# Kernel tuning notes

Hardware: AMD Instinct MI355X
Metric: run time of the kernel (lower is better)

The kernel has to match this reference:

```python
import jax, jax.numpy as jnp
import numpy as np

# RPE constants from the source: pix_per_patch=200//16, alpha=12, beta=24, gamma=96, num_buckets=49
ALPHA, BETA, GAMMA, PPP = 12.0, 24.0, 96.0, 12.0
NUM_BUCKETS = 49
LN_EPS = 1e-5


def _layernorm(x, w, b):
    m = jnp.mean(x, axis=-1, keepdims=True)
    v = jnp.mean((x - m) ** 2, axis=-1, keepdims=True)
    return (x - m) / jnp.sqrt(v + LN_EPS) * w + b


def _bucket_ids(ct):
    # ct: (B,T,2) int coords -> piecewise_index bucket ids shifted by beta, (B,T,T) int32
    ctf = ct.astype(jnp.float32)
    diff = ctf[:, :, None, :] - ctf[:, None, :, :]          # (B,T,T,2)
    dist = jnp.sqrt(jnp.sum(diff * diff, axis=-1))           # euclidean distance
    rel = jnp.trunc(dist / PPP)                              # torch.div(..., rounding_mode='trunc')
    abs_r = jnp.abs(rel)
    log_branch = jnp.sign(rel) * jnp.minimum(
        jnp.round(ALPHA + jnp.log(jnp.maximum(abs_r, 1e-6) / ALPHA) / np.log(GAMMA / ALPHA) * (BETA - ALPHA)),
        BETA)
    idx = jnp.where(abs_r <= ALPHA, jnp.round(rel), log_branch).astype(jnp.int32)
    return idx + int(BETA)                                   # shift into [0, num_buckets)


def setup_inputs() -> dict:
    key = jax.random.key(0)
    ks = jax.random.split(key, 12)
    B, T, C, H = 32, 500, 512, 8
    s = 0.02
    return {
        "x": jax.random.normal(ks[0], (B, T, C), jnp.float32),
        "ct": jax.random.randint(ks[1], (B, T, 2), 0, 200, jnp.int32),
        "w_attn": jax.random.normal(ks[2], (C, 3 * C), jnp.float32) * s,
        "b_attn": jnp.zeros((3 * C,), jnp.float32),
        "w_proj": jax.random.normal(ks[3], (C, C), jnp.float32) * s,
        "b_proj": jnp.zeros((C,), jnp.float32),
        "rpe_table": jax.random.normal(ks[4], (H, NUM_BUCKETS), jnp.float32) * s,
        "ln1_w": jnp.ones((C,), jnp.float32),
        "ln1_b": jnp.zeros((C,), jnp.float32),
        "ln2_w": jnp.ones((C,), jnp.float32),
        "ln2_b": jnp.zeros((C,), jnp.float32),
        "w_fc": jax.random.normal(ks[5], (C, 2 * C), jnp.float32) * s,
        "b_fc": jnp.zeros((2 * C,), jnp.float32),
        "w_fc2": jax.random.normal(ks[6], (2 * C, C), jnp.float32) * s,
        "b_fc2": jnp.zeros((C,), jnp.float32),
    }


def reference(x, ct, w_attn, b_attn, w_proj, b_proj, rpe_table,
              ln1_w, ln1_b, ln2_w, ln2_b, w_fc, b_fc, w_fc2, b_fc2):
    B, T, C = x.shape
    H = rpe_table.shape[0]
    D = C // H

    # --- RPEAttention ---
    bucket = _bucket_ids(ct)                                  # (B,T,T) int32 in [0,49)
    qkv = x @ w_attn + b_attn                                 # (B,T,3C)
    q, k, v = jnp.split(qkv, 3, axis=-1)
    q = q.reshape(B, T, H, D).transpose(0, 2, 1, 3)           # (B,H,T,D)
    k = k.reshape(B, T, H, D).transpose(0, 2, 1, 3)
    v = v.reshape(B, T, H, D).transpose(0, 2, 1, 3)
    att = jnp.einsum('bhtd,bhsd->bhts', q, k) * (1.0 / np.sqrt(D))
    # bias buffer is all ones -> masked_fill(bias==0) is a no-op
    # faithful replication of torch: table[:, flat].view(B,H,T,T) (a raw reshape of (H, B*T*T))
    rpe = rpe_table[:, bucket.reshape(-1)].reshape(B, H, T, T)
    att = jax.nn.softmax(att + rpe, axis=-1)
    y = jnp.einsum('bhts,bhsd->bthd', att, v).reshape(B, T, C)
    y = y @ w_proj + b_proj

    # --- Block: residual + LN, MLP (GELU exact), residual + LN ---
    x = _layernorm(x + y, ln1_w, ln1_b)
    h = jax.nn.gelu(x @ w_fc + b_fc, approximate=False)
    x = _layernorm(x + (h @ w_fc2 + b_fc2), ln2_w, ln2_b)
    return x
```

## Files before the change

### kernel.cpp

```cpp
#include <hip/hip_runtime.h>
#include <cstdint>
#include <cstddef>


typedef unsigned short ushort_t;
typedef __bf16 bf16x8 __attribute__((ext_vector_type(8)));
typedef float floatx4 __attribute__((ext_vector_type(4)));
typedef unsigned short ushort4v __attribute__((ext_vector_type(4)));
typedef unsigned short ushort8v __attribute__((ext_vector_type(8)));

#define DEV __device__ __forceinline__

#define B_ 32
#define T_ 500
#define C_ 512
#define H_ 8
#define M_ 16000

#define OFF_QK     0ULL
#define OFF_XBF    32800768ULL
#define OFF_BUCKET 49184768ULL
#define OFF_VT     57376768ULL
#define OFF_Y      74153984ULL
#define OFF_WATTN  90537984ULL
#define OFF_WPROJ  92110848ULL
#define OFF_WFC    92635136ULL
#define OFF_WFC2   93683712ULL
#define VT_BYTES   16777216ULL

DEV ushort_t f2bf(float f) {
  union { float f; unsigned u; } v; v.f = f;
  unsigned r = v.u + 0x7fffu + ((v.u >> 16) & 1u);
  return (ushort_t)(r >> 16);
}
DEV float bf2f(ushort_t u) {
  union { unsigned u; float f; } v; v.u = ((unsigned)u) << 16;
  return v.f;
}

DEV void gload16(const void* g, void* l) {
  __builtin_amdgcn_global_load_lds(
      (__attribute__((address_space(1))) void*)(g),
      (__attribute__((address_space(3))) void*)(l), 16, 0, 0);
}

__global__ __launch_bounds__(256) void cvt_bf16(const float* __restrict__ in,
                                                ushort_t* __restrict__ out, int n) {
  int i = (blockIdx.x * 256 + threadIdx.x) * 4;
  if (i >= n) return;
  float4 v = *(const float4*)(in + i);
  ushort4v o = { f2bf(v.x), f2bf(v.y), f2bf(v.z), f2bf(v.w) };
  *(ushort4v*)(out + i) = o;
}

struct WTDesc { const float* w; ushort_t* wt; int K; int N; };
struct WTArgs { WTDesc d[4]; };

__global__ __launch_bounds__(256) void wtrans_all(WTArgs a) {
  const int bid = blockIdx.x;
  int z, local;
  if (bid < 768)       { z = 0; local = bid; }
  else if (bid < 1024) { z = 1; local = bid - 768; }
  else if (bid < 1536) { z = 2; local = bid - 1024; }
  else                 { z = 3; local = bid - 1536; }
  const WTDesc dd = a.d[z];
  const int gx = dd.N >> 5;
  const int n0 = (local % gx) * 32, k0 = (local / gx) * 32;

  __shared__ float tile[32][33];
  const int c = threadIdx.x & 31, r = threadIdx.x >> 5;
#pragma unroll
  for (int rr = 0; rr < 4; ++rr)
    tile[r + rr * 8][c] = dd.w[(size_t)(k0 + r + rr * 8) * dd.N + n0 + c];
  __syncthreads();
#pragma unroll
  for (int rr = 0; rr < 4; ++rr)
    dd.wt[(size_t)(n0 + r + rr * 8) * dd.K + k0 + c] = f2bf(tile[c][r + rr * 8]);
}

__global__ __launch_bounds__(256) void bucket_kernel(const int* __restrict__ ct,
                                                     unsigned char* __restrict__ bucket) {
  const int b = blockIdx.y;
  const int tid = threadIdx.x, w = tid >> 6, lane = tid & 63;
  __shared__ int2 ctS[500];
  for (int j = tid; j < T_; j += 256) ctS[j] = ((const int2*)ct)[(size_t)b * T_ + j];
  __syncthreads();
  const int t = blockIdx.x * 4 + w;
  const int2 a = ctS[t];
  const float ax = (float)a.x, ay = (float)a.y;
  const size_t rowbase = (size_t)(b * T_ + t) << 9;
#pragma unroll
  for (int it = 0; it < 8; ++it) {
    const int s = it * 64 + lane;
    if (s < T_) {
      const int2 c2 = ctS[s];
      const float dx = ax - (float)c2.x, dy = ay - (float)c2.y;
      const float dist = __builtin_amdgcn_sqrtf(dx * dx + dy * dy);
      const float rel = truncf(dist * (1.0f / 12.0f));
      const float far = fminf(
          rintf(fmaf(__builtin_amdgcn_logf(rel * (1.0f / 12.0f)), 4.0f, 12.0f)), 24.0f);
      const float idx = (rel <= 12.0f) ? rel : far;
      bucket[rowbase + (s >> 6) * 64 + (s & 15) * 4 + ((s >> 4) & 3)]
          = (unsigned char)((int)idx + 24);
    }
  }
}

__global__ __launch_bounds__(256, 2)
void gemm_qkv(const ushort_t* __restrict__ A,
              const ushort_t* __restrict__ Bt,
              const float* __restrict__ bias,
              ushort_t* __restrict__ qk,
              ushort_t* __restrict__ vt) {
  constexpr int K = 512;
  const int bid = blockIdx.x;
  const int xcd = bid & 7, k = bid >> 3;
  const int n_blk = k % 12, mg = k / 12;
  const int m_blk = mg * 8 + xcd;
  if (m_blk >= 125) return;
  const int m0 = m_blk * 128, n0 = n_blk * 128;

  __shared__ __align__(16) ushort_t As[128 * 64];
  __shared__ __align__(16) ushort_t Bs[128 * 64];
  const int tid = threadIdx.x;
  const int lane = tid & 63, w = tid >> 6;
  const int wm = w >> 1, wn = w & 1;
  const int quad = lane >> 4, l15 = lane & 15;

  floatx4 acc[4][4] = {};

  for (int k0 = 0; k0 < K; k0 += 64) {
    __syncthreads();
#pragma unroll
    for (int j = 0; j < 4; ++j) {
      const int chunk = j * 256 + tid;
      const int row = chunk >> 3, pos = chunk & 7, c = pos ^ (row & 7);
      gload16(A + (size_t)(m0 + row) * K + k0 + c * 8, (char*)As + j * 4096 + w * 1024);
      gload16(Bt + (size_t)(n0 + row) * K + k0 + c * 8, (char*)Bs + j * 4096 + w * 1024);
    }
    asm volatile("s_waitcnt vmcnt(0)" ::: "memory");
    __syncthreads();

#pragma unroll
    for (int kq = 0; kq < 2; ++kq) {
      bf16x8 af[4], bfr[4];
#pragma unroll
      for (int t = 0; t < 4; ++t) {
        const int rowa = wm * 64 + t * 16 + l15;
        const int posa = (kq * 4 + quad) ^ (rowa & 7);
        af[t] = *(const bf16x8*)((const char*)As + rowa * 128 + posa * 16);
        const int rowb = wn * 64 + t * 16 + l15;
        const int posb = (kq * 4 + quad) ^ (rowb & 7);
        bfr[t] = *(const bf16x8*)((const char*)Bs + rowb * 128 + posb * 16);
      }
#pragma unroll
      for (int tm = 0; tm < 4; ++tm)
#pragma unroll
        for (int tn = 0; tn < 4; ++tn)
          acc[tm][tn] = __builtin_amdgcn_mfma_f32_16x16x32_bf16(af[tm], bfr[tn], acc[tm][tn], 0, 0, 0);
    }
  }

  if (n0 < 1024) {
#pragma unroll
    for (int tn = 0; tn < 4; ++tn) {
      const int n = n0 + wn * 64 + tn * 16 + l15;
      const float bs = bias[n];
#pragma unroll
      for (int tm = 0; tm < 4; ++tm)
#pragma unroll
        for (int r = 0; r < 4; ++r) {
          const int m = m0 + wm * 64 + tm * 16 + quad * 4 + r;
          qk[(size_t)m * 1024 + n] = f2bf(acc[tm][tn][r] + bs);
        }
    }
  } else {
#pragma unroll
    for (int tn = 0; tn < 4; ++tn) {
      const int n = n0 + wn * 64 + tn * 16 + l15;
      const float bs = bias[n];
      const int hh = (n >> 6) - 16, dd = n & 63;
#pragma unroll
      for (int tm = 0; tm < 4; ++tm) {
        const int mb = m0 + wm * 64 + tm * 16 + quad * 4;
        const int bb = mb / 500;
        const int ss = mb - bb * 500;
        ushort4v pk;
#pragma unroll
        for (int r = 0; r < 4; ++r) pk[r] = f2bf(acc[tm][tn][r] + bs);
        *(ushort4v*)(vt + (((size_t)(bb * 8 + hh)) * 64 + dd) * 512 + ss) = pk;
      }
    }
  }
}

template <int TN, int EPI>
__global__ __launch_bounds__(256, TN == 64 ? 4 : 2)
void gemm_bt(const ushort_t* __restrict__ A,
             const ushort_t* __restrict__ Bt,
             const float* __restrict__ bias,
             const float* __restrict__ resf,
             const ushort_t* __restrict__ resb,
             void* __restrict__ outp,
             int N, int K) {
  constexpr int TMW = (TN == 128) ? 4 : 2;
  const int nn = N / TN;
  const int bid = blockIdx.x;
  const int xcd = bid & 7, kk = bid >> 3;
  const int n_blk = kk % nn, mg = kk / nn;
  const int m_blk = mg * 8 + xcd;
  if (m_blk >= 125) return;
  const int m0 = m_blk * 128, n0 = n_blk * TN;

  __shared__ __align__(16) ushort_t As[128 * 64];
  __shared__ __align__(16) ushort_t Bs[TN * 64];
  const int tid = threadIdx.x;
  const int lane = tid & 63, w = tid >> 6;
  const int wm = (TN == 128) ? (w >> 1) : w;
  const int wn = (TN == 128) ? (w & 1) : 0;
  const int quad = lane >> 4, l15 = lane & 15;

  floatx4 acc[TMW][4] = {};

  for (int k0 = 0; k0 < K; k0 += 64) {
    __syncthreads();
#pragma unroll
    for (int j = 0; j < 4; ++j) {
      const int chunk = j * 256 + tid;
      const int row = chunk >> 3, pos = chunk & 7, c = pos ^ (row & 7);
      gload16(A + (size_t)(m0 + row) * K + k0 + c * 8, (char*)As + j * 4096 + w * 1024);
    }
#pragma unroll
    for (int j = 0; j < TN / 32; ++j) {
      const int chunk = j * 256 + tid;
      const int row = chunk >> 3, pos = chunk & 7, c = pos ^ (row & 7);
      gload16(Bt + (size_t)(n0 + row) * K + k0 + c * 8, (char*)Bs + j * 4096 + w * 1024);
    }
    asm volatile("s_waitcnt vmcnt(0)" ::: "memory");
    __syncthreads();

#pragma unroll
    for (int kq = 0; kq < 2; ++kq) {
      bf16x8 af[TMW], bfr[4];
#pragma unroll
      for (int t = 0; t < TMW; ++t) {
        const int row = wm * (TMW * 16) + t * 16 + l15;
        const int pos = (kq * 4 + quad) ^ (row & 7);
        af[t] = *(const bf16x8*)((const char*)As + row * 128 + pos * 16);
      }
#pragma unroll
      for (int t = 0; t < 4; ++t) {
        const int row = wn * 64 + t * 16 + l15;
        const int pos = (kq * 4 + quad) ^ (row & 7);
        bfr[t] = *(const bf16x8*)((const char*)Bs + row * 128 + pos * 16);
      }
#pragma unroll
      for (int tm = 0; tm < TMW; ++tm)
#pragma unroll
        for (int tn = 0; tn < 4; ++tn)
          acc[tm][tn] = __builtin_amdgcn_mfma_f32_16x16x32_bf16(af[tm], bfr[tn], acc[tm][tn], 0, 0, 0);
    }
  }

#pragma unroll
  for (int tn = 0; tn < 4; ++tn) {
    const int n = n0 + wn * 64 + tn * 16 + l15;
    const float bs = bias[n];
#pragma unroll
    for (int tm = 0; tm < TMW; ++tm) {
#pragma unroll
      for (int r = 0; r < 4; ++r) {
        const int m = m0 + wm * (TMW * 16) + tm * 16 + quad * 4 + r;
        const float v = acc[tm][tn][r] + bs;
        if (EPI == 1) {
          const float gv = 0.5f * v * (1.0f + erff(v * 0.70710678118654752f));
          ((ushort_t*)outp)[(size_t)m * N + n] = f2bf(gv);
        } else if (EPI == 2) {
          ((float*)outp)[(size_t)m * N + n] = v + resf[(size_t)m * N + n];
        } else {
          ((float*)outp)[(size_t)m * N + n] = v + bf2f(resb[(size_t)m * N + n]);
        }
      }
    }
  }
}

template <bool LAST>
DEV void attn_tile(const ushort_t* __restrict__ Ksb,
                   const ushort_t* __restrict__ VTsb,
                   char* pw, const unsigned* bw,
                   const bf16x8* qf, floatx4* o, float* lsum,
                   float treg, int quad, int l15) {
  floatx4 sc[4];
  __builtin_amdgcn_s_setprio(1);
#pragma unroll
  for (int tn = 0; tn < 4; ++tn) {
    floatx4 z = {0.0f, 0.0f, 0.0f, 0.0f};
#pragma unroll
    for (int kq = 0; kq < 2; ++kq) {
      const int row = tn * 16 + l15;
      const int pos = (kq * 4 + quad) ^ (row & 7);
      const bf16x8 kf = *(const bf16x8*)((const char*)Ksb + row * 128 + pos * 16);
      z = __builtin_amdgcn_mfma_f32_16x16x32_bf16(qf[kq], kf, z, 0, 0, 0);
    }
    sc[tn] = z;
  }
  __builtin_amdgcn_s_setprio(0);

#pragma unroll
  for (int r = 0; r < 4; ++r) {
    const int prow = quad * 4 + r;
#pragma unroll
    for (int tn = 0; tn < 4; ++tn) {
      const int idx4 = (int)((bw[r] >> (tn * 8)) & 63u) * 4;
      const float tv = __builtin_bit_cast(float,
          __builtin_amdgcn_ds_bpermute(idx4, __builtin_bit_cast(int, treg)));
      float p = __builtin_amdgcn_exp2f(fmaf(sc[tn][r], 0.18033688f, tv));
      if (LAST && (tn * 16 + l15 >= 52)) p = 0.0f;
      lsum[r] += p;
      const int chunk = (tn * 2 + (l15 >> 3)) ^ (prow & 7);
      *(ushort_t*)(pw + prow * 128 + chunk * 16 + (l15 & 7) * 2) =
          (ushort_t)(__builtin_bit_cast(unsigned, p) >> 16);
    }
  }
  asm volatile("" ::: "memory");

  __builtin_amdgcn_s_setprio(1);
#pragma unroll
  for (int ks = 0; ks < 2; ++ks) {
    const int ppos = (ks * 4 + quad) ^ (l15 & 7);
    const bf16x8 pfr = *(const bf16x8*)(pw + l15 * 128 + ppos * 16);
#pragma unroll
    for (int nd = 0; nd < 4; ++nd) {
      const int row = nd * 16 + l15;
      const int pos = (ks * 4 + quad) ^ (row & 7);
      const bf16x8 vf = *(const bf16x8*)((const char*)VTsb + row * 128 + pos * 16);
      o[nd] = __builtin_amdgcn_mfma_f32_16x16x32_bf16(pfr, vf, o[nd], 0, 0, 0);
    }
  }
  __builtin_amdgcn_s_setprio(0);
}

__global__ __launch_bounds__(256, 4) void attn_kernel(const ushort_t* __restrict__ qk,
                                                      const ushort_t* __restrict__ vt,
                                                      const unsigned char* __restrict__ bucket,
                                                      const float* __restrict__ rpe,
                                                      ushort_t* __restrict__ y) {
  const int bid = blockIdx.x;
  const int xcd = bid & 7, sl = bid >> 3;
  const int qt = sl & 7;
  const int pair = xcd * 32 + (sl >> 3);
  const int h = pair >> 5, b = pair & 31;
  const int g = b >> 2;
  const int bpp = 8 * (b & 3) + h;

  __shared__ __align__(16) ushort_t Qs[64 * 64];
  __shared__ __align__(16) ushort_t Ks[2][64 * 64];
  __shared__ __align__(16) ushort_t VTs[2][64 * 64];

  const int tid = threadIdx.x;
  const int lane = tid & 63, w = tid >> 6;
  const int quad = lane >> 4, l15 = lane & 15;
  const int t0 = qt * 64;

#pragma unroll
  for (int j = 0; j < 2; ++j) {
    const int chunk = j * 256 + tid;
    const int row = chunk >> 3, pos = chunk & 7, c = pos ^ (row & 7);
    gload16(qk + (size_t)(b * T_ + t0 + row) * 1024 + h * 64 + c * 8,
            (char*)Qs + j * 4096 + w * 1024);
    gload16(qk + (size_t)(b * T_ + row) * 1024 + 512 + h * 64 + c * 8,
            (char*)Ks[0] + j * 4096 + w * 1024);
    gload16(vt + ((size_t)(b * 8 + h) * 64 + row) * 512 + c * 8,
            (char*)VTs[0] + j * 4096 + w * 1024);
  }

  const float treg = rpe[g * 49 + (lane < 49 ? lane : 48)] * 1.44269504f;

  const unsigned char* bkbase[4];
#pragma unroll
  for (int r = 0; r < 4; ++r) {
    const int tr = t0 + w * 16 + quad * 4 + r;
    const int trc = (tr < T_) ? tr : (T_ - 1);
    bkbase[r] = bucket + ((size_t)(bpp * T_ + trc) << 9) + (l15 << 2);
  }
  unsigned bw[4];
#pragma unroll
  for (int r = 0; r < 4; ++r) bw[r] = *(const unsigned*)(bkbase[r]);

  asm volatile("s_waitcnt vmcnt(0)" ::: "memory");
  __syncthreads();

  bf16x8 qf[2];
#pragma unroll
  for (int kq = 0; kq < 2; ++kq) {
    const int row = w * 16 + l15;
    const int pos = (kq * 4 + quad) ^ (row & 7);
    qf[kq] = *(const bf16x8*)((const char*)Qs + row * 128 + pos * 16);
  }

  floatx4 o[4] = {};
  float lsum[4] = {0.0f, 0.0f, 0.0f, 0.0f};
  char* pw = (char*)Qs + w * 2048;

#pragma unroll 1
  for (int st = 0; st < 7; ++st) {
    const int cb = st & 1, nb = cb ^ 1;
    const int s0n = (st + 1) * 64;
#pragma unroll
    for (int j = 0; j < 2; ++j) {
      const int chunk = j * 256 + tid;
      const int row = chunk >> 3, pos = chunk & 7, c = pos ^ (row & 7);
      gload16(qk + (size_t)(b * T_ + s0n + row) * 1024 + 512 + h * 64 + c * 8,
              (char*)Ks[nb] + j * 4096 + w * 1024);
      gload16(vt + ((size_t)(b * 8 + h) * 64 + row) * 512 + s0n + c * 8,
              (char*)VTs[nb] + j * 4096 + w * 1024);
    }
    unsigned bwn[4];
#pragma unroll
    for (int r = 0; r < 4; ++r) bwn[r] = *(const unsigned*)(bkbase[r] + s0n);

    attn_tile<false>(Ks[cb], VTs[cb], pw, bw, qf, o, lsum, treg, quad, l15);

    asm volatile("s_waitcnt vmcnt(0)" ::: "memory");
    __syncthreads();
#pragma unroll
    for (int r = 0; r < 4; ++r) bw[r] = bwn[r];
  }
  attn_tile<true>(Ks[1], VTs[1], pw, bw, qf, o, lsum, treg, quad, l15);

#pragma unroll
  for (int r = 0; r < 4; ++r) {
    float s = lsum[r];
    s += __shfl_xor(s, 1);
    s += __shfl_xor(s, 2);
    s += __shfl_xor(s, 4);
    s += __shfl_xor(s, 8);
    const int t = t0 + w * 16 + quad * 4 + r;
    if (t < T_) {
      const float inv = 1.0f / s;
#pragma unroll
      for (int nd = 0; nd < 4; ++nd)
        y[((size_t)b * T_ + t) * 512 + h * 64 + nd * 16 + l15] = f2bf(o[nd][r] * inv);
    }
  }
}

__global__ __launch_bounds__(256) void ln_kernel(const float* z,
                                                 const float* __restrict__ gw,
                                                 const float* __restrict__ gb,
                                                 ushort_t* out_bf, float* out_f) {
  const int tid = threadIdx.x, lane = tid & 63, w = tid >> 6;
  const int row = blockIdx.x * 4 + w;
  const float* zr = z + (size_t)row * 512;
  const int c0 = lane * 8;
  const float4 v0 = *(const float4*)(zr + c0);
  const float4 v1 = *(const float4*)(zr + c0 + 4);
  float s = ((v0.x + v0.y) + (v0.z + v0.w)) + ((v1.x + v1.y) + (v1.z + v1.w));
#pragma unroll
  for (int m = 1; m < 64; m <<= 1) s += __shfl_xor(s, m);
  const float mean = s * (1.0f / 512.0f);
  float d[8] = { v0.x - mean, v0.y - mean, v0.z - mean, v0.w - mean,
                 v1.x - mean, v1.y - mean, v1.z - mean, v1.w - mean };
  float q = 0.0f;
#pragma unroll
  for (int j = 0; j < 8; ++j) q += d[j] * d[j];
#pragma unroll
  for (int m = 1; m < 64; m <<= 1) q += __shfl_xor(q, m);
  const float rstd = rsqrtf(q * (1.0f / 512.0f) + 1e-5f);
  const float4 ga = *(const float4*)(gw + c0);
  const float4 gc = *(const float4*)(gw + c0 + 4);
  const float4 ba = *(const float4*)(gb + c0);
  const float4 bc = *(const float4*)(gb + c0 + 4);
  float ov[8];
  ov[0] = d[0] * rstd * ga.x + ba.x;
  ov[1] = d[1] * rstd * ga.y + ba.y;
  ov[2] = d[2] * rstd * ga.z + ba.z;
  ov[3] = d[3] * rstd * ga.w + ba.w;
  ov[4] = d[4] * rstd * gc.x + bc.x;
  ov[5] = d[5] * rstd * gc.y + bc.y;
  ov[6] = d[6] * rstd * gc.z + bc.z;
  ov[7] = d[7] * rstd * gc.w + bc.w;
  if (out_bf) {
    ushort8v pk;
#pragma unroll
    for (int j = 0; j < 8; ++j) pk[j] = f2bf(ov[j]);
    *(ushort8v*)(out_bf + (size_t)row * 512 + c0) = pk;
  }
  if (out_f) {
    float4 o0 = { ov[0], ov[1], ov[2], ov[3] };
    float4 o1 = { ov[4], ov[5], ov[6], ov[7] };
    *(float4*)(out_f + (size_t)row * 512 + c0) = o0;
    *(float4*)(out_f + (size_t)row * 512 + c0 + 4) = o1;
  }
}

extern "C" void kernel_launch(void* const* d_in, const int* in_sizes, int n_in,
                              void* d_out, int out_size, void* d_ws, size_t ws_size,
                              hipStream_t stream) {
  (void)in_sizes; (void)n_in; (void)out_size; (void)ws_size;
  const float* x      = (const float*)d_in[0];
  const int*   ct     = (const int*)d_in[1];
  const float* w_attn = (const float*)d_in[2];
  const float* b_attn = (const float*)d_in[3];
  const float* w_proj = (const float*)d_in[4];
  const float* b_proj = (const float*)d_in[5];
  const float* rpe    = (const float*)d_in[6];
  const float* ln1w   = (const float*)d_in[7];
  const float* ln1b   = (const float*)d_in[8];
  const float* ln2w   = (const float*)d_in[9];
  const float* ln2b   = (const float*)d_in[10];
  const float* w_fc   = (const float*)d_in[11];
  const float* b_fc   = (const float*)d_in[12];
  const float* w_fc2  = (const float*)d_in[13];
  const float* b_fc2  = (const float*)d_in[14];
  float* out = (float*)d_out;

  char* ws = (char*)d_ws;
  ushort_t* qk      = (ushort_t*)(ws + OFF_QK);
  ushort_t* h_buf   = (ushort_t*)(ws + OFF_QK);
  ushort_t* x_bf    = (ushort_t*)(ws + OFF_XBF);
  ushort_t* x1      = (ushort_t*)(ws + OFF_XBF);
  unsigned char* bk = (unsigned char*)(ws + OFF_BUCKET);
  ushort_t* vt      = (ushort_t*)(ws + OFF_VT);
  ushort_t* y       = (ushort_t*)(ws + OFF_Y);
  ushort_t* wt_attn = (ushort_t*)(ws + OFF_WATTN);
  ushort_t* wt_proj = (ushort_t*)(ws + OFF_WPROJ);
  ushort_t* wt_fc   = (ushort_t*)(ws + OFF_WFC);
  ushort_t* wt_fc2  = (ushort_t*)(ws + OFF_WFC2);

  cvt_bf16<<<dim3(8000), 256, 0, stream>>>(x, x_bf, M_ * C_);
  WTArgs wta;
  wta.d[0] = { w_attn, wt_attn, 512, 1536 };
  wta.d[1] = { w_proj, wt_proj, 512, 512 };
  wta.d[2] = { w_fc,   wt_fc,   512, 1024 };
  wta.d[3] = { w_fc2,  wt_fc2,  1024, 512 };
  wtrans_all<<<dim3(2048), 256, 0, stream>>>(wta);
  bucket_kernel<<<dim3(125, 32), 256, 0, stream>>>(ct, bk);
  hipMemsetAsync(vt, 0, VT_BYTES, stream);

  gemm_qkv<<<dim3(1536), 256, 0, stream>>>(x_bf, wt_attn, b_attn, qk, vt);
  attn_kernel<<<dim3(2048), 256, 0, stream>>>(qk, vt, bk, rpe, y);
  gemm_bt<64, 2><<<dim3(1024), 256, 0, stream>>>(y, wt_proj, b_proj, x, nullptr, out, 512, 512);
  ln_kernel<<<dim3(4000), 256, 0, stream>>>(out, ln1w, ln1b, x1, nullptr);
  gemm_bt<128, 1><<<dim3(1024), 256, 0, stream>>>(x1, wt_fc, b_fc, nullptr, nullptr, h_buf, 1024, 512);
  gemm_bt<64, 3><<<dim3(1024), 256, 0, stream>>>(h_buf, wt_fc2, b_fc2, nullptr, x1, out, 512, 1024);
  ln_kernel<<<dim3(4000), 256, 0, stream>>>(out, ln2w, ln2b, nullptr, out);
}
```

Before: 298.9 us.

## Enlarge attention query tile to 128 rows with 512 threads and single-buffered V

The attention kernel now processes 128 query rows per block with 8 waves instead of 64 rows with 4 waves, halving the grid so each K/V tile is loaded once for twice as many queries. V is single-buffered and loaded mid-tile, with a barrier between the softmax and PV phases. Bucket bytes are pre-shifted by 2 so the bpermute index needs no multiply. The extra block-wide barriers and the V load landing just before use may expose latency in exchange for less global traffic and LDS.

```diff
diff --git a/kernel.cpp b/kernel.cpp
--- a/kernel.cpp
+++ b/kernel.cpp
@@ -101,7 +101,7 @@
           rintf(fmaf(__builtin_amdgcn_logf(rel * (1.0f / 12.0f)), 4.0f, 12.0f)), 24.0f);
       const float idx = (rel <= 12.0f) ? rel : far;
       bucket[rowbase + (s >> 6) * 64 + (s & 15) * 4 + ((s >> 4) & 3)]
-          = (unsigned char)((int)idx + 24);
+          = (unsigned char)(((int)idx + 24) << 2);
     }
   }
 }
@@ -287,7 +287,7 @@
 
 template <bool LAST>
 DEV void attn_tile(const ushort_t* __restrict__ Ksb,
-                   const ushort_t* __restrict__ VTsb,
+                   const ushort_t* __restrict__ Vsb,
                    char* pw, const unsigned* bw,
                    const bf16x8* qf, floatx4* o, float* lsum,
                    float treg, int quad, int l15) {
@@ -312,7 +312,7 @@
     const int prow = quad * 4 + r;
 #pragma unroll
     for (int tn = 0; tn < 4; ++tn) {
-      const int idx4 = (int)((bw[r] >> (tn * 8)) & 63u) * 4;
+      const int idx4 = (int)((bw[r] >> (tn * 8)) & 255u);
       const float tv = __builtin_bit_cast(float,
           __builtin_amdgcn_ds_bpermute(idx4, __builtin_bit_cast(int, treg)));
       float p = __builtin_amdgcn_exp2f(fmaf(sc[tn][r], 0.18033688f, tv));
@@ -323,7 +323,9 @@
           (ushort_t)(__builtin_bit_cast(unsigned, p) >> 16);
     }
   }
-  asm volatile("" ::: "memory");
+
+  asm volatile("s_waitcnt vmcnt(0)" ::: "memory");
+  __syncthreads();
 
   __builtin_amdgcn_s_setprio(1);
 #pragma unroll
@@ -334,46 +336,46 @@
     for (int nd = 0; nd < 4; ++nd) {
       const int row = nd * 16 + l15;
       const int pos = (ks * 4 + quad) ^ (row & 7);
-      const bf16x8 vf = *(const bf16x8*)((const char*)VTsb + row * 128 + pos * 16);
+      const bf16x8 vf = *(const bf16x8*)((const char*)Vsb + row * 128 + pos * 16);
       o[nd] = __builtin_amdgcn_mfma_f32_16x16x32_bf16(pfr, vf, o[nd], 0, 0, 0);
     }
   }
   __builtin_amdgcn_s_setprio(0);
 }
 
-__global__ __launch_bounds__(256, 4) void attn_kernel(const ushort_t* __restrict__ qk,
+__global__ __launch_bounds__(512, 8) void attn_kernel(const ushort_t* __restrict__ qk,
                                                       const ushort_t* __restrict__ vt,
                                                       const unsigned char* __restrict__ bucket,
                                                       const float* __restrict__ rpe,
                                                       ushort_t* __restrict__ y) {
   const int bid = blockIdx.x;
   const int xcd = bid & 7, sl = bid >> 3;
-  const int qt = sl & 7;
-  const int pair = xcd * 32 + (sl >> 3);
+  const int qt = sl & 3;
+  const int pair = xcd * 32 + (sl >> 2);
   const int h = pair >> 5, b = pair & 31;
   const int g = b >> 2;
   const int bpp = 8 * (b & 3) + h;
 
-  __shared__ __align__(16) ushort_t Qs[64 * 64];
+  __shared__ __align__(16) ushort_t Qs[128 * 64];
   __shared__ __align__(16) ushort_t Ks[2][64 * 64];
-  __shared__ __align__(16) ushort_t VTs[2][64 * 64];
+  __shared__ __align__(16) ushort_t Vs[64 * 64];
 
   const int tid = threadIdx.x;
   const int lane = tid & 63, w = tid >> 6;
   const int quad = lane >> 4, l15 = lane & 15;
-  const int t0 = qt * 64;
+  const int t0 = qt * 128;
+
+  const int srow = tid >> 3, spos = tid & 7, scol = spos ^ (srow & 7);
 
 #pragma unroll
   for (int j = 0; j < 2; ++j) {
-    const int chunk = j * 256 + tid;
+    const int chunk = j * 512 + tid;
     const int row = chunk >> 3, pos = chunk & 7, c = pos ^ (row & 7);
     gload16(qk + (size_t)(b * T_ + t0 + row) * 1024 + h * 64 + c * 8,
-            (char*)Qs + j * 4096 + w * 1024);
-    gload16(qk + (size_t)(b * T_ + row) * 1024 + 512 + h * 64 + c * 8,
-            (char*)Ks[0] + j * 4096 + w * 1024);
-    gload16(vt + ((size_t)(b * 8 + h) * 64 + row) * 512 + c * 8,
-            (char*)VTs[0] + j * 4096 + w * 1024);
-  }
+            (char*)Qs + j * 8192 + w * 1024);
+  }
+  gload16(qk + (size_t)(b * T_ + srow) * 1024 + 512 + h * 64 + scol * 8,
+          (char*)Ks[0] + w * 1024);
 
   const float treg = rpe[g * 49 + (lane < 49 ? lane : 48)] * 1.44269504f;
 
@@ -405,29 +407,25 @@
 
 #pragma unroll 1
   for (int st = 0; st < 7; ++st) {
-    const int cb = st & 1, nb = cb ^ 1;
-    const int s0n = (st + 1) * 64;
-#pragma unroll
-    for (int j = 0; j < 2; ++j) {
-      const int chunk = j * 256 + tid;
-      const int row = chunk >> 3, pos = chunk & 7, c = pos ^ (row & 7);
-      gload16(qk + (size_t)(b * T_ + s0n + row) * 1024 + 512 + h * 64 + c * 8,
-              (char*)Ks[nb] + j * 4096 + w * 1024);
-      gload16(vt + ((size_t)(b * 8 + h) * 64 + row) * 512 + s0n + c * 8,
-              (char*)VTs[nb] + j * 4096 + w * 1024);
-    }
+    const int cb = st & 1;
+    __syncthreads();
+    gload16(vt + ((size_t)(b * 8 + h) * 64 + srow) * 512 + st * 64 + scol * 8,
+            (char*)Vs + w * 1024);
+    gload16(qk + (size_t)(b * T_ + (st + 1) * 64 + srow) * 1024 + 512 + h * 64 + scol * 8,
+            (char*)Ks[cb ^ 1] + w * 1024);
     unsigned bwn[4];
 #pragma unroll
-    for (int r = 0; r < 4; ++r) bwn[r] = *(const unsigned*)(bkbase[r] + s0n);
-
-    attn_tile<false>(Ks[cb], VTs[cb], pw, bw, qf, o, lsum, treg, quad, l15);
-
-    asm volatile("s_waitcnt vmcnt(0)" ::: "memory");
-    __syncthreads();
+    for (int r = 0; r < 4; ++r) bwn[r] = *(const unsigned*)(bkbase[r] + (st + 1) * 64);
+
+    attn_tile<false>(Ks[cb], Vs, pw, bw, qf, o, lsum, treg, quad, l15);
+
 #pragma unroll
     for (int r = 0; r < 4; ++r) bw[r] = bwn[r];
   }
-  attn_tile<true>(Ks[1], VTs[1], pw, bw, qf, o, lsum, treg, quad, l15);
+  __syncthreads();
+  gload16(vt + ((size_t)(b * 8 + h) * 64 + srow) * 512 + 448 + scol * 8,
+          (char*)Vs + w * 1024);
+  attn_tile<true>(Ks[1], Vs, pw, bw, qf, o, lsum, treg, quad, l15);
 
 #pragma unroll
   for (int r = 0; r < 4; ++r) {
@@ -540,7 +538,7 @@
   hipMemsetAsync(vt, 0, VT_BYTES, stream);
 
   gemm_qkv<<<dim3(1536), 256, 0, stream>>>(x_bf, wt_attn, b_attn, qk, vt);
-  attn_kernel<<<dim3(2048), 256, 0, stream>>>(qk, vt, bk, rpe, y);
+  attn_kernel<<<dim3(1024), 512, 0, stream>>>(qk, vt, bk, rpe, y);
   gemm_bt<64, 2><<<dim3(1024), 256, 0, stream>>>(y, wt_proj, b_proj, x, nullptr, out, 512, 512);
   ln_kernel<<<dim3(4000), 256, 0, stream>>>(out, ln1w, ln1b, x1, nullptr);
   gemm_bt<128, 1><<<dim3(1024), 256, 0, stream>>>(x1, wt_fc, b_fc, nullptr, nullptr, h_buf, 1024, 512);
```

After: 365.9 us. 1.22x slower.
